# Kernel optimization log

Measured on AMD Instinct MI355X. Metric: run time of the kernel, lower is better.

## Reference

```python
import jax, jax.numpy as jnp
import numpy as np

B, N, D = 4, 1024, 512
H = 8
HD = D // H  # 64
EPS = 1e-12  # F.normalize eps


def _l2_normalize(t):
    # torch.nn.functional.normalize(p=2, dim=-1): x / max(||x||_2, eps)
    nrm = jnp.sqrt(jnp.sum(t * t, axis=-1, keepdims=True))
    return t / jnp.maximum(nrm, EPS)


def setup_inputs() -> dict:
    key = jax.random.key(0)
    ks = jax.random.split(key, 5)
    scale = 1.0 / np.sqrt(D)
    inp = {
        "x": jax.random.normal(ks[0], (B, N, D), dtype=jnp.float32),
        "Wq": jax.random.normal(ks[1], (D, D), dtype=jnp.float32) * scale,
        "Wk": jax.random.normal(ks[2], (D, D), dtype=jnp.float32) * scale,
        "Wv": jax.random.normal(ks[3], (D, D), dtype=jnp.float32) * scale,
        "Wo": jax.random.normal(ks[4], (D, D), dtype=jnp.float32) * scale,
        "bq": jnp.zeros((D,), dtype=jnp.float32),
        "bk": jnp.zeros((D,), dtype=jnp.float32),
        "bv": jnp.zeros((D,), dtype=jnp.float32),
        "bo": jnp.zeros((D,), dtype=jnp.float32),
    }
    return inp


def reference(x, Wq, Wk, Wv, Wo, bq, bk, bv, bo):
    b, n, d = x.shape
    # projections (nn.Linear: x @ W.T + b), split heads -> (b, h, n, hd)
    def split_heads(t):
        return t.reshape(b, n, H, HD).transpose(0, 2, 1, 3)

    q = split_heads(x @ Wq.T + bq)
    k = split_heads(x @ Wk.T + bk)
    v = split_heads(x @ Wv.T + bv)

    q = _l2_normalize(jax.nn.elu(q))
    k = _l2_normalize(jax.nn.elu(k))

    # causal linear attention: running prefix sum of k (outer) v states
    kv_step = jnp.einsum('bhnd,bhne->bhnde', k, v)      # (b,h,n,hd,hd)
    kv_prefix = jnp.cumsum(kv_step, axis=2)             # causal prefix state
    out = jnp.einsum('bhnd,bhnde->bhne', q, kv_prefix)  # (b,h,n,hd)

    out = out.transpose(0, 2, 1, 3).reshape(b, n, d)
    return out @ Wo.T + bo
```

## Files before the change

kernel.cpp:

```cpp
#include <hip/hip_runtime.h>
#include <cmath>

#define BB 4
#define NN 1024
#define DD 512
#define HH 8
#define HDIM 64
#define ROWS (BB * NN)
#define NCHUNK 16
#define KA 512
#define WMAT ((size_t)512 * 512)

typedef _Float16 f16;
typedef f16   f16x8 __attribute__((ext_vector_type(8)));
typedef f16   f16x4 __attribute__((ext_vector_type(4)));
typedef float f32x4 __attribute__((ext_vector_type(4)));

#define GLOAD_LDS16(g, l) \
    __builtin_amdgcn_global_load_lds((const __attribute__((address_space(1))) void*)(g), \
                                     (__attribute__((address_space(3))) void*)(l), 16, 0, 0)

__global__ __launch_bounds__(256)
void split_all(const float* __restrict__ x,
               const float* __restrict__ Wq, const float* __restrict__ Wk,
               const float* __restrict__ Wv, const float* __restrict__ Wo,
               f16* __restrict__ xa, f16* __restrict__ wa)
{
    const int bid = blockIdx.x;
    const float* src;
    f16* dstbase;
    int t;
    if (bid < 2048) {
        t = bid * 256 + threadIdx.x;
        src = x;
        dstbase = xa;
    } else {
        int wb = bid - 2048;
        int m  = wb >> 8;
        t = (wb & 255) * 256 + threadIdx.x;
        src = (m == 0) ? Wq : (m == 1) ? Wk : (m == 2) ? Wv : Wo;
        dstbase = wa + (size_t)m * WMAT;
    }
    float4 v = ((const float4*)src)[t];
    int r = t >> 7;
    int c = (t & 127) * 4;
    f16x4 h;
    h[0] = (f16)v.x; h[1] = (f16)v.y; h[2] = (f16)v.z; h[3] = (f16)v.w;
    *(f16x4*)(dstbase + (size_t)r * 512 + c) = h;
}

template<int OUTMODE>
__global__ __launch_bounds__(256)
void mm_f16(const f16* __restrict__ A, const f16* __restrict__ Wm,
            const float* __restrict__ b0, const float* __restrict__ b1,
            const float* __restrict__ b2,
            f16* __restrict__ qf, f16* __restrict__ kf,
            f16* __restrict__ ktb, f16* __restrict__ vtb,
            float* __restrict__ obase)
{
    constexpr int BN = (OUTMODE == 0) ? 128 : 64;
    constexpr int NW = BN / 32;
    constexpr int BR = BN / 32;

    __shared__ __align__(16) f16 As[128 * 64];
    __shared__ __align__(16) f16 Bs[BN * 64];

    const int t    = threadIdx.x;
    const int lane = t & 63;
    const int wid  = t >> 6;
    const int wr   = wid >> 1;
    const int wc   = wid & 1;
    const int l16  = lane & 15;
    const int g16  = lane >> 4;

    const int nwg = 32 * gridDim.y;
    const int lin = blockIdx.y * 32 + blockIdx.x;
    const int swz = (lin & 7) * (nwg >> 3) + (lin >> 3);
    const int bx  = swz & 31;
    const int by  = swz >> 5;

    const int r0 = bx * 128;
    const int c0 = by * BN;
    const int z  = (OUTMODE == 0) ? (c0 >> 9) : 0;
    const int cw = (OUTMODE == 0) ? (c0 & 511) : c0;

    const f16* Wz = Wm + (size_t)z * WMAT;

    f32x4 acc[4][NW] = {};

    for (int kt = 0; kt < 8; ++kt) {
        const int kb = kt * 64;
        #pragma unroll
        for (int i = 0; i < 4; ++i) {
            int f = i * 256 + t;
            int row = f >> 3;
            int sc  = (f & 7) ^ (row & 7);
            GLOAD_LDS16(A + (size_t)(r0 + row) * KA + kb + sc * 8, As + f * 8);
        }
        #pragma unroll
        for (int i = 0; i < BR; ++i) {
            int f = i * 256 + t;
            int row = f >> 3;
            int sc  = (f & 7) ^ (row & 7);
            GLOAD_LDS16(Wz + (size_t)(cw + row) * KA + kb + sc * 8, Bs + f * 8);
        }
        __syncthreads();

        #pragma unroll
        for (int kk = 0; kk < 2; ++kk) {
            f16x8 af[4], bfr[NW];
            #pragma unroll
            for (int mi = 0; mi < 4; ++mi) {
                int lr = wr * 64 + mi * 16 + l16;
                int sc = (kk * 4 + g16) ^ (lr & 7);
                af[mi] = *(const f16x8*)(As + lr * 64 + sc * 8);
            }
            #pragma unroll
            for (int ni = 0; ni < NW; ++ni) {
                int lr = wc * (BN / 2) + ni * 16 + l16;
                int sc = (kk * 4 + g16) ^ (lr & 7);
                bfr[ni] = *(const f16x8*)(Bs + lr * 64 + sc * 8);
            }
            #pragma unroll
            for (int mi = 0; mi < 4; ++mi)
                #pragma unroll
                for (int ni = 0; ni < NW; ++ni)
                    acc[mi][ni] = __builtin_amdgcn_mfma_f32_16x16x32_f16(af[mi], bfr[ni], acc[mi][ni], 0, 0, 0);
        }
        __syncthreads();
    }

    if (OUTMODE == 1) {
        #pragma unroll
        for (int mi = 0; mi < 4; ++mi)
            #pragma unroll
            for (int ni = 0; ni < NW; ++ni) {
                int cg = c0 + wc * (BN / 2) + ni * 16 + l16;
                float bv = b0[cg];
                #pragma unroll
                for (int r = 0; r < 4; ++r) {
                    int rg = r0 + wr * 64 + mi * 16 + g16 * 4 + r;
                    obase[(size_t)rg * DD + cg] = acc[mi][ni][r] + bv;
                }
            }
    } else {
        const float* bias = (z == 0) ? b0 : (z == 1) ? b1 : b2;

        #pragma unroll
        for (int mi = 0; mi < 4; ++mi)
            #pragma unroll
            for (int ni = 0; ni < NW; ++ni) {
                float bv = bias[cw + wc * 64 + ni * 16 + l16];
                #pragma unroll
                for (int r = 0; r < 4; ++r) {
                    float v = acc[mi][ni][r] + bv;
                    if (z < 2) v = (v > 0.f) ? v : expm1f(v);
                    acc[mi][ni][r] = v;
                }
            }
        if (z < 2) {
            #pragma unroll
            for (int mi = 0; mi < 4; ++mi)
                #pragma unroll
                for (int r = 0; r < 4; ++r) {
                    float ss = 0.f;
                    #pragma unroll
                    for (int ni = 0; ni < NW; ++ni) ss += acc[mi][ni][r] * acc[mi][ni][r];
                    ss += __shfl_xor(ss, 1);
                    ss += __shfl_xor(ss, 2);
                    ss += __shfl_xor(ss, 4);
                    ss += __shfl_xor(ss, 8);
                    float sc = 1.f / fmaxf(sqrtf(ss), 1e-12f);
                    #pragma unroll
                    for (int ni = 0; ni < NW; ++ni) acc[mi][ni][r] *= sc;
                }
        }

        const int h = (cw >> 6) + wc;
        const int b = r0 >> 10;

        if (z <= 1) {
            f16* plane = (z == 0) ? qf : kf;
            #pragma unroll
            for (int mi = 0; mi < 4; ++mi)
                #pragma unroll
                for (int r = 0; r < 4; ++r) {
                    int rg = r0 + wr * 64 + mi * 16 + g16 * 4 + r;
                    f16* dst = plane + ((size_t)(b * HH + h) * NN + (rg & 1023)) * HDIM;
                    #pragma unroll
                    for (int ni = 0; ni < NW; ++ni) dst[ni * 16 + l16] = (f16)acc[mi][ni][r];
                }
        }

        if (z >= 1) {
            f16* tb = (z == 1) ? ktb : vtb;
            f16* T = (wid < 2) ? (As + wid * 4096) : (Bs + (wid - 2) * 4096);
            #pragma unroll
            for (int mi = 0; mi < 4; ++mi)
                #pragma unroll
                for (int ni = 0; ni < NW; ++ni)
                    #pragma unroll
                    for (int r = 0; r < 4; ++r) {
                        int n_ = mi * 16 + g16 * 4 + r;
                        int d_ = ni * 16 + l16;
                        *(f16*)((char*)T + d_ * 128 + (((n_ >> 3) ^ (d_ & 7)) * 16) + (n_ & 7) * 2)
                            = (f16)acc[mi][ni][r];
                    }
            __syncthreads();
            const int n0 = (r0 & 1023) + wr * 64;
            #pragma unroll
            for (int p = 0; p < 8; ++p) {
                int d_ = p * 8 + (lane >> 3);
                int ck = lane & 7;
                f16x8 v8 = *(const f16x8*)((char*)T + d_ * 128 + ((ck ^ (d_ & 7)) * 16));
                *(f16x8*)(tb + ((size_t)(b * HH + h) * HDIM + d_) * NN + n0 + ck * 8) = v8;
            }
        }
    }
}

__global__ __launch_bounds__(256)
void state_prefix(const f16* __restrict__ ktb, const f16* __restrict__ vtb,
                  f16* __restrict__ ptb)
{
    __shared__ __align__(16) f16 Kt[2][64 * 64];
    __shared__ __align__(16) f16 Vt[2][64 * 64];
    __shared__ __align__(16) f16 PtL[16 * 64];

    const int bh = blockIdx.x;
    const int eq = blockIdx.y;
    const int t  = threadIdx.x;
    const int lane = t & 63;
    const int wid  = t >> 6;
    const int l16  = lane & 15;
    const int g16  = lane >> 4;

    auto stage = [&](int ch, int buf) {
        #pragma unroll
        for (int i = 0; i < 2; ++i) {
            int f = i * 256 + t;
            int row = f >> 3;
            int sc  = (f & 7) ^ (row & 7);
            GLOAD_LDS16(ktb + ((size_t)bh * HDIM + row) * NN + ch * 64 + sc * 8, Kt[buf] + f * 8);
            GLOAD_LDS16(vtb + ((size_t)bh * HDIM + row) * NN + ch * 64 + sc * 8, Vt[buf] + f * 8);
        }
    };

    float pref[4] = {};
    const int d = wid * 16 + l16;

    stage(0, 0);

    for (int ch = 0; ch < NCHUNK; ++ch) {
        const int buf = ch & 1;
        stage(ch < 15 ? ch + 1 : 15, buf ^ 1);

        #pragma unroll
        for (int r = 0; r < 4; ++r) {
            int e = g16 * 4 + r;
            *(f16*)((char*)PtL + e * 128 + (((d >> 3) ^ (e & 7)) * 16) + (d & 7) * 2)
                = (f16)pref[r];
        }

        asm volatile("s_waitcnt vmcnt(4)" ::: "memory");
        asm volatile("s_waitcnt lgkmcnt(0)" ::: "memory");
        __builtin_amdgcn_s_barrier();
        __builtin_amdgcn_sched_barrier(0);

        {
            f16x4 v4 = *(const f16x4*)(PtL + t * 4);
            *(f16x4*)(ptb + (size_t)(bh * NCHUNK + ch) * 4096 + eq * 1024 + t * 4) = v4;
        }

        f32x4 sacc = {};
        #pragma unroll
        for (int ks = 0; ks < 2; ++ks) {
            int ra = eq * 16 + l16;
            f16x8 av = *(const f16x8*)(Vt[buf] + ra * 64 + ((ks * 4 + g16) ^ (ra & 7)) * 8);
            int rb = wid * 16 + l16;
            f16x8 bv = *(const f16x8*)(Kt[buf] + rb * 64 + ((ks * 4 + g16) ^ (rb & 7)) * 8);
            sacc = __builtin_amdgcn_mfma_f32_16x16x32_f16(av, bv, sacc, 0, 0, 0);
        }
        #pragma unroll
        for (int r = 0; r < 4; ++r) pref[r] += sacc[r];

        __builtin_amdgcn_s_barrier();
    }
}

__global__ __launch_bounds__(256)
void attn_chunk(const f16* __restrict__ qf, const f16* __restrict__ kf,
                const f16* __restrict__ vtb, const f16* __restrict__ ptb,
                f16* __restrict__ aug)
{
    __shared__ __align__(16) f16 Qs[64 * 64];
    __shared__ __align__(16) f16 Ks[64 * 64];
    __shared__ __align__(16) f16 Vt[64 * 64];
    __shared__ __align__(16) f16 Pt[64 * 64];
    __shared__ __align__(16) f16 Ss[64 * 64];

    const int bh = blockIdx.x;
    const int ch = blockIdx.y;
    const int t  = threadIdx.x;
    const int lane = t & 63;
    const int wid  = t >> 6;
    const int wr   = wid >> 1;
    const int wc   = wid & 1;
    const int l16  = lane & 15;
    const int g16  = lane >> 4;

    #pragma unroll
    for (int i = 0; i < 2; ++i) {
        int f = i * 256 + t;
        int row = f >> 3;
        int sc  = (f & 7) ^ (row & 7);
        GLOAD_LDS16(qf  + ((size_t)bh * NN + ch * 64 + row) * HDIM + sc * 8, Qs + f * 8);
        GLOAD_LDS16(kf  + ((size_t)bh * NN + ch * 64 + row) * HDIM + sc * 8, Ks + f * 8);
        GLOAD_LDS16(vtb + ((size_t)bh * HDIM + row) * NN + ch * 64 + sc * 8, Vt + f * 8);
        GLOAD_LDS16(ptb + (size_t)(bh * NCHUNK + ch) * 4096 + f * 8, Pt + f * 8);
    }
    __syncthreads();

    f32x4 sacc[2][2] = {};
    #pragma unroll
    for (int ks = 0; ks < 2; ++ks) {
        f16x8 af[2], bfr[2];
        #pragma unroll
        for (int mi = 0; mi < 2; ++mi) {
            int row = wr * 32 + mi * 16 + l16;
            int sc  = (ks * 4 + g16) ^ (row & 7);
            af[mi] = *(const f16x8*)(Qs + row * 64 + sc * 8);
        }
        #pragma unroll
        for (int ni = 0; ni < 2; ++ni) {
            int row = wc * 32 + ni * 16 + l16;
            int sc  = (ks * 4 + g16) ^ (row & 7);
            bfr[ni] = *(const f16x8*)(Ks + row * 64 + sc * 8);
        }
        #pragma unroll
        for (int mi = 0; mi < 2; ++mi)
            #pragma unroll
            for (int ni = 0; ni < 2; ++ni)
                sacc[mi][ni] = __builtin_amdgcn_mfma_f32_16x16x32_f16(af[mi], bfr[ni], sacc[mi][ni], 0, 0, 0);
    }
    #pragma unroll
    for (int mi = 0; mi < 2; ++mi)
        #pragma unroll
        for (int ni = 0; ni < 2; ++ni)
            #pragma unroll
            for (int r = 0; r < 4; ++r) {
                int i = wr * 32 + mi * 16 + g16 * 4 + r;
                int j = wc * 32 + ni * 16 + l16;
                float v = (j <= i) ? sacc[mi][ni][r] : 0.f;
                *(f16*)((char*)Ss + i * 128 + (((j >> 3) ^ (i & 7)) * 16) + (j & 7) * 2) = (f16)v;
            }
    __syncthreads();

    f32x4 oacc[2][2] = {};
    #pragma unroll
    for (int ks = 0; ks < 2; ++ks) {
        f16x8 af[2], bfr[2];
        #pragma unroll
        for (int mi = 0; mi < 2; ++mi) {
            int row = wr * 32 + mi * 16 + l16;
            int sc  = (ks * 4 + g16) ^ (row & 7);
            af[mi] = *(const f16x8*)(Qs + row * 64 + sc * 8);
        }
        #pragma unroll
        for (int ni = 0; ni < 2; ++ni) {
            int row = wc * 32 + ni * 16 + l16;
            int sc  = (ks * 4 + g16) ^ (row & 7);
            bfr[ni] = *(const f16x8*)(Pt + row * 64 + sc * 8);
        }
        #pragma unroll
        for (int mi = 0; mi < 2; ++mi)
            #pragma unroll
            for (int ni = 0; ni < 2; ++ni)
                oacc[mi][ni] = __builtin_amdgcn_mfma_f32_16x16x32_f16(af[mi], bfr[ni], oacc[mi][ni], 0, 0, 0);
    }
    #pragma unroll
    for (int ks = 0; ks < 2; ++ks) {
        f16x8 af[2], bfr[2];
        #pragma unroll
        for (int mi = 0; mi < 2; ++mi) {
            int row = wr * 32 + mi * 16 + l16;
            int sc  = (ks * 4 + g16) ^ (row & 7);
            af[mi] = *(const f16x8*)(Ss + row * 64 + sc * 8);
        }
        #pragma unroll
        for (int ni = 0; ni < 2; ++ni) {
            int row = wc * 32 + ni * 16 + l16;
            int sc  = (ks * 4 + g16) ^ (row & 7);
            bfr[ni] = *(const f16x8*)(Vt + row * 64 + sc * 8);
        }
        #pragma unroll
        for (int mi = 0; mi < 2; ++mi)
            #pragma unroll
            for (int ni = 0; ni < 2; ++ni)
                oacc[mi][ni] = __builtin_amdgcn_mfma_f32_16x16x32_f16(af[mi], bfr[ni], oacc[mi][ni], 0, 0, 0);
    }

    const int b = bh >> 3;
    const int h = bh & 7;
    #pragma unroll
    for (int mi = 0; mi < 2; ++mi)
        #pragma unroll
        for (int ni = 0; ni < 2; ++ni)
            #pragma unroll
            for (int r = 0; r < 4; ++r) {
                int i = wr * 32 + mi * 16 + g16 * 4 + r;
                int e = wc * 32 + ni * 16 + l16;
                aug[((size_t)(b * NN + ch * 64 + i)) * KA + h * HDIM + e] = (f16)oacc[mi][ni][r];
            }
}

extern "C" void kernel_launch(void* const* d_in, const int* in_sizes, int n_in,
                              void* d_out, int out_size, void* d_ws, size_t ws_size,
                              hipStream_t stream)
{
    (void)in_sizes; (void)n_in; (void)out_size; (void)ws_size;

    const float* x  = (const float*)d_in[0];
    const float* Wq = (const float*)d_in[1];
    const float* Wk = (const float*)d_in[2];
    const float* Wv = (const float*)d_in[3];
    const float* Wo = (const float*)d_in[4];
    const float* bq = (const float*)d_in[5];
    const float* bk = (const float*)d_in[6];
    const float* bv = (const float*)d_in[7];
    const float* bo = (const float*)d_in[8];
    float* out = (float*)d_out;

    char* ws = (char*)d_ws;
    f16* qf  = (f16*)(ws);
    f16* kf  = (f16*)(ws + (size_t)4  * 1024 * 1024);
    f16* ktb = (f16*)(ws + (size_t)8  * 1024 * 1024);
    f16* vtb = (f16*)(ws + (size_t)12 * 1024 * 1024);
    f16* ptb = (f16*)(ws + (size_t)16 * 1024 * 1024);
    f16* xa  = (f16*)(ws + (size_t)20 * 1024 * 1024);
    f16* aug = (f16*)(ws + (size_t)24 * 1024 * 1024);
    f16* wa  = (f16*)(ws + (size_t)28 * 1024 * 1024);

    dim3 blk(256);

    split_all<<<dim3(3072), blk, 0, stream>>>(x, Wq, Wk, Wv, Wo, xa, wa);

    mm_f16<0><<<dim3(32, 12), blk, 0, stream>>>(xa, wa, bq, bk, bv, qf, kf, ktb, vtb, nullptr);

    state_prefix<<<dim3(32, 4), blk, 0, stream>>>(ktb, vtb, ptb);
    attn_chunk<<<dim3(32, NCHUNK), blk, 0, stream>>>(qf, kf, vtb, ptb, aug);

    mm_f16<1><<<dim3(32, 8), blk, 0, stream>>>(aug, wa + (size_t)3 * WMAT, bo, nullptr, nullptr,
                                               nullptr, nullptr, nullptr, nullptr, out);
}
```

Before: 60.46 us.

## Double-buffer LDS tiles in f16 GEMM to overlap global loads with MFMA

Splits the A and B shared-memory tiles into two buffers and issues the next k-tile's global-to-LDS loads before computing on the current one. A manual s_waitcnt vmcnt leaves only the newer batch of loads outstanding, and raw s_barrier replaces __syncthreads. The goal is to hide global memory latency behind the matrix math. It doubles LDS use, which may lower occupancy, and the hand-tuned vmcnt counts must match the number of loads issued per stage.

```diff
diff --git a/kernel.cpp b/kernel.cpp
--- a/kernel.cpp
+++ b/kernel.cpp
@@ -62,8 +62,8 @@
     constexpr int NW = BN / 32;
     constexpr int BR = BN / 32;
 
-    __shared__ __align__(16) f16 As[128 * 64];
-    __shared__ __align__(16) f16 Bs[BN * 64];
+    __shared__ __align__(16) f16 As[2][128 * 64];
+    __shared__ __align__(16) f16 Bs[2][BN * 64];
 
     const int t    = threadIdx.x;
     const int lane = t & 63;
@@ -86,25 +86,39 @@
 
     const f16* Wz = Wm + (size_t)z * WMAT;
 
-    f32x4 acc[4][NW] = {};
-
-    for (int kt = 0; kt < 8; ++kt) {
+    auto stage = [&](int buf, int kt) {
         const int kb = kt * 64;
         #pragma unroll
         for (int i = 0; i < 4; ++i) {
             int f = i * 256 + t;
             int row = f >> 3;
             int sc  = (f & 7) ^ (row & 7);
-            GLOAD_LDS16(A + (size_t)(r0 + row) * KA + kb + sc * 8, As + f * 8);
+            GLOAD_LDS16(A + (size_t)(r0 + row) * KA + kb + sc * 8, As[buf] + f * 8);
         }
         #pragma unroll
         for (int i = 0; i < BR; ++i) {
             int f = i * 256 + t;
             int row = f >> 3;
             int sc  = (f & 7) ^ (row & 7);
-            GLOAD_LDS16(Wz + (size_t)(cw + row) * KA + kb + sc * 8, Bs + f * 8);
-        }
-        __syncthreads();
+            GLOAD_LDS16(Wz + (size_t)(cw + row) * KA + kb + sc * 8, Bs[buf] + f * 8);
+        }
+    };
+
+    f32x4 acc[4][NW] = {};
+
+    stage(0, 0);
+
+    for (int kt = 0; kt < 8; ++kt) {
+        const int buf = kt & 1;
+        if (kt < 7) {
+            stage(buf ^ 1, kt + 1);
+            if (OUTMODE == 0) asm volatile("s_waitcnt vmcnt(8)" ::: "memory");
+            else              asm volatile("s_waitcnt vmcnt(6)" ::: "memory");
+        } else {
+            asm volatile("s_waitcnt vmcnt(0)" ::: "memory");
+        }
+        __builtin_amdgcn_s_barrier();
+        __builtin_amdgcn_sched_barrier(0);
 
         #pragma unroll
         for (int kk = 0; kk < 2; ++kk) {
@@ -113,13 +127,13 @@
             for (int mi = 0; mi < 4; ++mi) {
                 int lr = wr * 64 + mi * 16 + l16;
                 int sc = (kk * 4 + g16) ^ (lr & 7);
-                af[mi] = *(const f16x8*)(As + lr * 64 + sc * 8);
+                af[mi] = *(const f16x8*)(As[buf] + lr * 64 + sc * 8);
             }
             #pragma unroll
             for (int ni = 0; ni < NW; ++ni) {
                 int lr = wc * (BN / 2) + ni * 16 + l16;
                 int sc = (kk * 4 + g16) ^ (lr & 7);
-                bfr[ni] = *(const f16x8*)(Bs + lr * 64 + sc * 8);
+                bfr[ni] = *(const f16x8*)(Bs[buf] + lr * 64 + sc * 8);
             }
             #pragma unroll
             for (int mi = 0; mi < 4; ++mi)
@@ -127,7 +141,7 @@
                 for (int ni = 0; ni < NW; ++ni)
                     acc[mi][ni] = __builtin_amdgcn_mfma_f32_16x16x32_f16(af[mi], bfr[ni], acc[mi][ni], 0, 0, 0);
         }
-        __syncthreads();
+        __builtin_amdgcn_s_barrier();
     }
 
     if (OUTMODE == 1) {
@@ -194,7 +208,7 @@
 
         if (z >= 1) {
             f16* tb = (z == 1) ? ktb : vtb;
-            f16* T = (wid < 2) ? (As + wid * 4096) : (Bs + (wid - 2) * 4096);
+            f16* T = (wid < 2) ? (As[0] + wid * 4096) : (Bs[0] + (wid - 2) * 4096);
             #pragma unroll
             for (int mi = 0; mi < 4; ++mi)
                 #pragma unroll
```

Result: faster. 56.57 us (-6.4%).
